# Performance work log

Measured on AMD Instinct MI355X. Metric: run time of the kernel, lower is better.

Reference implementation:

```python
import jax, jax.numpy as jnp
import numpy as np

B = 32768   # batch (agents)
H = 64      # h_dim
E = 16      # embedding_dim
M = 6       # num_modes (n_samples)
P = M * 2   # traj_points
T = 30      # pred_len (seq_len)


def setup_inputs() -> dict:
    key = jax.random.key(0)
    ks = jax.random.split(key, 14)
    def s(k, shape, scale=0.1):
        return jax.random.normal(k, shape, jnp.float32) * scale
    return dict(
        traj_abs=s(ks[0], (1, B, 2), 1.0),
        traj_rel=s(ks[1], (1, B, 2), 1.0),
        h0=s(ks[2], (1, B, H)),
        c0=s(ks[3], (1, B, H)),
        W_ih=s(ks[4], (4 * H, E)),
        W_hh=s(ks[5], (4 * H, H)),
        b_ih=s(ks[6], (4 * H,)),
        b_hh=s(ks[7], (4 * H,)),
        W_se=s(ks[8], (E, P)),
        b_se=s(ks[9], (E,)),
        W_pos=s(ks[10], (P, H)),
        b_pos=s(ks[11], (P,)),
        W_conf=s(ks[12], (M, H)),
        b_conf=s(ks[13], (M,)),
    )


def reference(traj_abs, traj_rel, h0, c0, W_ih, W_hh, b_ih, b_hh,
              W_se, b_se, W_pos, b_pos, W_conf, b_conf):
    b = traj_rel.shape[1]
    # repeat_interleave the (x,y) pair num_modes times along feature dim -> [b, 12]
    rel12 = jnp.tile(traj_rel.reshape(b, 1, 2), (1, M, 1)).reshape(b, P)
    x = jax.nn.leaky_relu(rel12 @ W_se.T + b_se)  # [b, E]
    h = h0[0]
    c = c0[0]

    def step(carry, _):
        x, h, c = carry
        # PyTorch LSTM cell, gate order i, f, g, o
        gates = x @ W_ih.T + b_ih + h @ W_hh.T + b_hh  # [b, 4H]
        i, f, g, o = jnp.split(gates, 4, axis=-1)
        c = jax.nn.sigmoid(f) * c + jax.nn.sigmoid(i) * jnp.tanh(g)
        h = jax.nn.sigmoid(o) * jnp.tanh(c)
        rel = h @ W_pos.T + b_pos                      # [b, P]
        x = jax.nn.leaky_relu(rel @ W_se.T + b_se)     # [b, E]
        return (x, h, c), rel

    (x, h, c), rels = jax.lax.scan(step, (x, h, c), None, length=T)  # rels: [T, b, P]
    pred = rels.reshape(T, b, M, 2).transpose(1, 2, 0, 3)            # [b, M, T, 2]
    conf = jax.nn.softmax(h @ W_conf.T + b_conf, axis=1)             # [b, M]
    return pred, conf
```

## Files before the change

kernel.cpp:

```cpp
#include <hip/hip_runtime.h>
#include <hip/hip_bf16.h>

typedef _Float16 half8 __attribute__((ext_vector_type(8)));
typedef _Float16 half4 __attribute__((ext_vector_type(4)));
typedef float float4v __attribute__((ext_vector_type(4)));

#define BATCH 32768
#define TT 30

#if __has_builtin(__builtin_amdgcn_exp2f)
#define FEXP2(x) __builtin_amdgcn_exp2f(x)
#else
#define FEXP2(x) __expf((x) * 0.6931471805599453f)
#endif
#if __has_builtin(__builtin_amdgcn_rcpf)
#define FRCP(x) __builtin_amdgcn_rcpf(x)
#else
#define FRCP(x) (1.0f / (x))
#endif

#define NLOG2E  -1.4426950408889634f
#define N2LOG2E -2.8853900817779268f

#define WFRAG_OFF 0
#define WCF_OFF   12288
#define BIASB_OFF 13312
#define SXY_OFF   13568
#define CBIAS_OFF 13616
#define WCONF_OFF 13648
#define BCONF_OFF 14032
#define FLAG_IDX  14038
#define CONF_BASE (BATCH * 360)

__global__ void detect_kernel(const unsigned short* __restrict__ raw,
                              int* __restrict__ flag_out) {
    __shared__ int sflag[256];
    int local = 0;
    for (int i = threadIdx.x; i < 16384; i += 256) {
        unsigned short u = raw[i];
        if ((u & 0x7F80u) == 0x7F80u) local = 1;
    }
    sflag[threadIdx.x] = local;
    __syncthreads();
    if (threadIdx.x == 0) {
        int f = 0;
        for (int i = 0; i < 256; ++i) f |= sflag[i];
        flag_out[0] = f;
    }
}

__device__ __forceinline__ float ldin(const void* p, int i, int isf32) {
    return isf32 ? ((const float*)p)[i]
                 : (float)((const __hip_bfloat16*)p)[i];
}

__global__ void prep_kernel(const void* __restrict__ W_ih,
                            const void* __restrict__ W_hh,
                            const void* __restrict__ b_ih,
                            const void* __restrict__ b_hh,
                            const void* __restrict__ W_se,
                            const void* __restrict__ b_se,
                            const void* __restrict__ W_pos,
                            const void* __restrict__ b_pos,
                            const void* __restrict__ W_conf,
                            const void* __restrict__ b_conf,
                            float* __restrict__ ws)
{
    const int isf32 = ((const int*)(ws + FLAG_IDX))[0];
    int tid = blockIdx.x * blockDim.x + threadIdx.x;
    int stride = gridDim.x * blockDim.x;
    _Float16* wfh = (_Float16*)ws;

    for (int idx = tid; idx < 24576; idx += stride) {
        int jj = idx & 7, r = idx >> 3;
        int lane = r & 63; r >>= 6;
        int ks = r % 3; r /= 3;
        int gate = r & 3; int wv = r >> 2;
        int col = lane & 15, akq = lane >> 4;
        int k = ks * 32 + akq * 8 + jj;
        int row = gate * 64 + wv * 16 + col;
        float v = 0.f;
        if (k < 16) v = ldin(W_ih, row * 16 + k, isf32);
        else if (k < 80) v = ldin(W_hh, row * 64 + (k - 16), isf32);
        v *= (gate == 2) ? N2LOG2E : NLOG2E;
        wfh[idx] = (_Float16)v;
    }
    _Float16* wch = (_Float16*)(ws + WCF_OFF);
    for (int idx = tid; idx < 2048; idx += stride) {
        int jj = idx & 7, r = idx >> 3;
        int lane = r & 63; r >>= 6;
        int ks = r & 1, role = r >> 1;
        int col = lane & 15, akq = lane >> 4;
        int k = ks * 32 + akq * 8 + jj;
        float v = 0.f;
        if (role == 0) {
            if (col < 12) v = ldin(W_pos, col * 64 + k, isf32);
        } else {
            float s = 0.f;
            for (int p = 0; p < 12; ++p)
                s += ldin(W_se, col * 12 + p, isf32) * ldin(W_pos, p * 64 + k, isf32);
            v = s;
        }
        wch[idx] = (_Float16)v;
    }
    for (int idx = tid; idx < 256; idx += stride) {
        int gate = idx >> 6;
        float scale = (gate == 2) ? N2LOG2E : NLOG2E;
        ws[BIASB_OFF + idx] = (ldin(b_ih, idx, isf32) + ldin(b_hh, idx, isf32)) * scale;
    }
    for (int idx = tid; idx < 16; idx += stride) {
        float sx = 0.f, sy = 0.f;
        for (int m = 0; m < 6; ++m) {
            sx += ldin(W_se, idx * 12 + 2 * m, isf32);
            sy += ldin(W_se, idx * 12 + 2 * m + 1, isf32);
        }
        ws[SXY_OFF + idx * 3 + 0] = sx;
        ws[SXY_OFF + idx * 3 + 1] = sy;
        ws[SXY_OFF + idx * 3 + 2] = ldin(b_se, idx, isf32);
    }
    for (int idx = tid; idx < 32; idx += stride) {
        int w = idx >> 4, cc = idx & 15;
        float v = 0.f;
        if (w == 0) {
            if (cc < 12) v = ldin(b_pos, cc, isf32);
        } else {
            float s = ldin(b_se, cc, isf32);
            for (int p = 0; p < 12; ++p)
                s += ldin(W_se, cc * 12 + p, isf32) * ldin(b_pos, p, isf32);
            v = s;
        }
        ws[CBIAS_OFF + idx] = v;
    }
    for (int idx = tid; idx < 384; idx += stride)
        ws[WCONF_OFF + idx] = ldin(W_conf, idx, isf32);
    for (int idx = tid; idx < 6; idx += stride)
        ws[BCONF_OFF + idx] = ldin(b_conf, idx, isf32);
}

__global__ __launch_bounds__(256, 4) void lstm_kernel(
    const void* __restrict__ traj_rel,
    const void* __restrict__ h0,
    const void* __restrict__ c0,
    const float* __restrict__ ws,
    float* __restrict__ out)
{
    __shared__ _Float16 zsh[2 * 16 * 104];
    __shared__ _Float16 predh[12 * 30 * 36];

    const int tid = threadIdx.x;
    const int lane = tid & 63;
    const int wid = __builtin_amdgcn_readfirstlane(tid >> 6);
    const int role = wid & 1;
    const int col16 = lane & 15;
    const int akq = lane >> 4;
    const int base = blockIdx.x * 32;
    const int isf32 = ((const int*)(ws + FLAG_IDX))[0];

    const float4v* wfg = (const float4v*)ws;
    half8 Bf[4][3];
#pragma unroll
    for (int tl = 0; tl < 4; ++tl)
#pragma unroll
        for (int ks = 0; ks < 3; ++ks)
            Bf[tl][ks] = __builtin_bit_cast(half8,
                wfg[((wid * 4 + tl) * 3 + ks) * 64 + lane]);
    float bias4[4];
#pragma unroll
    for (int tl = 0; tl < 4; ++tl)
        bias4[tl] = ws[BIASB_OFF + tl * 64 + wid * 16 + col16];
    half8 wfc[2];
    {
        const float4v* wcg = (const float4v*)(ws + WCF_OFF);
#pragma unroll
        for (int ks = 0; ks < 2; ++ks)
            wfc[ks] = __builtin_bit_cast(half8, wcg[(role * 2 + ks) * 64 + lane]);
    }
    const float cb = ws[CBIAS_OFF + role * 16 + col16];

    float cg0[4], cg1[4];
    {
        int unit = wid * 16 + col16;
#pragma unroll
        for (int i = 0; i < 4; ++i) {
            cg0[i] = ldin(c0, (base + akq * 4 + i) * 64 + unit, isf32);
            cg1[i] = ldin(c0, (base + 16 + akq * 4 + i) * 64 + unit, isf32);
        }
    }
    {
        int m = tid & 31, jq2 = tid >> 5;
        int g = m >> 4, row = m & 15;
        _Float16* zg = &zsh[g * 1664];
        half8 ha;
#pragma unroll
        for (int i = 0; i < 8; ++i)
            ha[i] = (_Float16)ldin(h0, (base + m) * 64 + jq2 * 8 + i, isf32);
        *(half8*)&zg[row * 104 + 16 + jq2 * 8] = ha;
        if (jq2 < 4) {
            float rx = ldin(traj_rel, 2 * (base + m), isf32);
            float ry = ldin(traj_rel, 2 * (base + m) + 1, isf32);
            half4 xs;
#pragma unroll
            for (int i = 0; i < 4; ++i) {
                int e = 4 * jq2 + i;
                float x = fmaf(rx, ws[SXY_OFF + e * 3],
                          fmaf(ry, ws[SXY_OFF + e * 3 + 1], ws[SXY_OFF + e * 3 + 2]));
                xs[i] = (_Float16)(x > 0.f ? x : 0.01f * x);
            }
            *(half4*)&zg[row * 104 + 4 * jq2] = xs;
        } else if (jq2 < 6) {
            half8 zz = {};
            *(half8*)&zg[row * 104 + 80 + (jq2 - 4) * 8] = zz;
        }
    }
    __syncthreads();

    const int zbA = col16 * 104 + akq * 8;
    const int zbC = zbA + 16;
    const int hwb = 16 + wid * 16 + col16;

    float4v acc0[4], acc1[4];

#define ZG(g) (&zsh[(g) * 1664])

#define PHASE_A(G, ACC) do {                                                  \
    _Float16* zg_ = ZG(G);                                                    \
    _Pragma("unroll")                                                         \
    for (int tl = 0; tl < 4; ++tl) {                                          \
        float bv = bias4[tl];                                                 \
        ACC[tl][0] = bv; ACC[tl][1] = bv; ACC[tl][2] = bv; ACC[tl][3] = bv;   \
    }                                                                         \
    _Pragma("unroll")                                                         \
    for (int ks = 0; ks < 3; ++ks) {                                          \
        half8 af_ = *(const half8*)&zg_[zbA + ks * 32];                       \
        _Pragma("unroll")                                                     \
        for (int tl = 0; tl < 4; ++tl)                                        \
            ACC[tl] = __builtin_amdgcn_mfma_f32_16x16x32_f16(                 \
                af_, Bf[tl][ks], ACC[tl], 0, 0, 0);                           \
    }                                                                         \
} while (0)

#define PHASE_B(G, ACC, CARR) do {                                            \
    _Float16* zg_ = ZG(G);                                                    \
    _Pragma("unroll")                                                         \
    for (int i = 0; i < 4; ++i) {                                             \
        float si = FRCP(1.0f + FEXP2(ACC[0][i]));                             \
        float sf = FRCP(1.0f + FEXP2(ACC[1][i]));                             \
        float tg = fmaf(2.0f, FRCP(1.0f + FEXP2(ACC[2][i])), -1.0f);          \
        float so = FRCP(1.0f + FEXP2(ACC[3][i]));                             \
        float cn = fmaf(sf, CARR[i], si * tg);                                \
        CARR[i] = cn;                                                         \
        float th = fmaf(2.0f, FRCP(1.0f + FEXP2(cn * N2LOG2E)), -1.0f);       \
        float hn = so * th;                                                   \
        zg_[(akq * 4 + i) * 104 + hwb] = (_Float16)hn;                        \
    }                                                                         \
} while (0)

#define PHASE_C(G, T) do {                                                    \
    _Float16* zg_ = ZG(G);                                                    \
    float4v racc_;                                                            \
    racc_[0] = cb; racc_[1] = cb; racc_[2] = cb; racc_[3] = cb;               \
    _Pragma("unroll")                                                         \
    for (int ks = 0; ks < 2; ++ks) {                                          \
        half8 af_ = *(const half8*)&zg_[zbC + ks * 32];                       \
        racc_ = __builtin_amdgcn_mfma_f32_16x16x32_f16(                       \
            af_, wfc[ks], racc_, 0, 0, 0);                                    \
    }                                                                         \
    if (role == 0) {                                                          \
        if (col16 < 12) {                                                     \
            half4 hv_;                                                        \
            _Pragma("unroll")                                                 \
            for (int i = 0; i < 4; ++i) hv_[i] = (_Float16)racc_[i];          \
            *(half4*)&predh[(col16 * 30 + (T)) * 36 + (G) * 16 + akq * 4] = hv_; \
        }                                                                     \
    } else if ((T) != TT - 1) {                                               \
        _Pragma("unroll")                                                     \
        for (int i = 0; i < 4; ++i) {                                         \
            float xv_ = racc_[i];                                             \
            xv_ = xv_ > 0.f ? xv_ : 0.01f * xv_;                              \
            zg_[(akq * 4 + i) * 104 + col16] = (_Float16)xv_;                 \
        }                                                                     \
    }                                                                         \
} while (0)

    PHASE_A(0, acc0);
    __syncthreads();
    PHASE_A(1, acc1); PHASE_B(0, acc0, cg0);
    __syncthreads();
    if (wid < 2) PHASE_C(0, 0);
    PHASE_B(1, acc1, cg1);
    __syncthreads();

    for (int t = 1; t < TT; ++t) {
        PHASE_A(0, acc0);
        if (wid >= 2) PHASE_C(1, t - 1);
        __syncthreads();
        PHASE_A(1, acc1); PHASE_B(0, acc0, cg0);
        __syncthreads();
        if (wid < 2) PHASE_C(0, t);
        PHASE_B(1, acc1, cg1);
        __syncthreads();
    }
    if (wid >= 2) PHASE_C(1, TT - 1);
    __syncthreads();

    {
        float4* po4 = (float4*)(out + (size_t)base * 360);
#pragma unroll 1
        for (int q2 = 0; q2 < 12; ++q2) {
            int idx4 = q2 * 256 + tid;
            if (idx4 < 2880) {
                int a = idx4 / 90, rem = idx4 % 90;
                int m = rem / 15, tq = rem % 15;
                int t0 = tq * 2;
                float4 o;
                o.x = (float)predh[((2 * m + 0) * 30 + t0) * 36 + a];
                o.y = (float)predh[((2 * m + 1) * 30 + t0) * 36 + a];
                o.z = (float)predh[((2 * m + 0) * 30 + t0 + 1) * 36 + a];
                o.w = (float)predh[((2 * m + 1) * 30 + t0 + 1) * 36 + a];
                po4[idx4] = o;
            }
        }
    }

    if (wid == 0 && lane < 32) {
        int m = lane;
        int g = m >> 4, row = m & 15;
        float l[6];
#pragma unroll
        for (int md = 0; md < 6; ++md) l[md] = ws[BCONF_OFF + md];
        for (int jj = 0; jj < 64; ++jj) {
            float hv = (float)zsh[g * 1664 + row * 104 + 16 + jj];
#pragma unroll
            for (int md = 0; md < 6; ++md)
                l[md] = fmaf(hv, ws[WCONF_OFF + md * 64 + jj], l[md]);
        }
        float mx = l[0];
#pragma unroll
        for (int md = 1; md < 6; ++md) mx = fmaxf(mx, l[md]);
        float ex[6], s = 0.f;
#pragma unroll
        for (int md = 0; md < 6; ++md) { ex[md] = __expf(l[md] - mx); s += ex[md]; }
        float inv = FRCP(s);
#pragma unroll
        for (int md = 0; md < 6; ++md)
            out[CONF_BASE + (size_t)(base + m) * 6 + md] = ex[md] * inv;
    }
}

extern "C" void kernel_launch(void* const* d_in, const int* in_sizes, int n_in,
                              void* d_out, int out_size, void* d_ws, size_t ws_size,
                              hipStream_t stream) {
    const void* traj_rel = d_in[1];
    const void* h0   = d_in[2];
    const void* c0   = d_in[3];
    const void* W_ih = d_in[4];
    const void* W_hh = d_in[5];
    const void* b_ih = d_in[6];
    const void* b_hh = d_in[7];
    const void* W_se = d_in[8];
    const void* b_se = d_in[9];
    const void* W_pos  = d_in[10];
    const void* b_pos  = d_in[11];
    const void* W_conf = d_in[12];
    const void* b_conf = d_in[13];
    float* ws = (float*)d_ws;
    float* out = (float*)d_out;

    detect_kernel<<<1, 256, 0, stream>>>((const unsigned short*)W_hh,
                                         (int*)(ws + FLAG_IDX));
    prep_kernel<<<40, 256, 0, stream>>>(W_ih, W_hh, b_ih, b_hh, W_se, b_se,
                                        W_pos, b_pos, W_conf, b_conf, ws);
    lstm_kernel<<<BATCH / 32, 256, 0, stream>>>(traj_rel, h0, c0, ws, out);
}
```

Baseline: 207.9 us.

## Double-buffer LSTM hidden state in LDS, fuse gate phases, and cut barriers per step

Each row of the shared z buffer now holds two hidden-state slots, so a step can write the new h into one slot while other waves still read the old h from the other. This lets the gate MFMA and the activation phase be fused into one PHASE_AB and removes one __syncthreads per timestep. The loop is unrolled by two to alternate slots. The activation math is also recombined to use fewer reciprocals by sharing denominators (sigmoid/tanh products folded into one rcp). The cost is a larger LDS footprint and more complex index arithmetic, plus some risk of overflow in the combined exponent products.

```diff
diff --git a/kernel.cpp b/kernel.cpp
--- a/kernel.cpp
+++ b/kernel.cpp
@@ -144,7 +144,7 @@
     const float* __restrict__ ws,
     float* __restrict__ out)
 {
-    __shared__ _Float16 zsh[2 * 16 * 104];
+    __shared__ _Float16 zsh[2 * 16 * 168];
     __shared__ _Float16 predh[12 * 30 * 36];
 
     const int tid = threadIdx.x;
@@ -177,6 +177,21 @@
     }
     const float cb = ws[CBIAS_OFF + role * 16 + col16];
 
+    int aoff[2][3];
+#pragma unroll
+    for (int p = 0; p < 2; ++p)
+#pragma unroll
+        for (int ks = 0; ks < 3; ++ks) {
+            int q = ks * 4 + akq;
+            int off = (q < 2) ? q * 8
+                    : (q < 10) ? 32 + p * 64 + (q - 2) * 8
+                               : 16 + (q - 10) * 8;
+            aoff[p][ks] = col16 * 168 + off;
+        }
+    const int zcb = col16 * 168 + 32 + akq * 8;
+    const int rb = akq * 672;
+    const int hb = 32 + wid * 16 + col16;
+
     float cg0[4], cg1[4];
     {
         int unit = wid * 16 + col16;
@@ -189,12 +204,12 @@
     {
         int m = tid & 31, jq2 = tid >> 5;
         int g = m >> 4, row = m & 15;
-        _Float16* zg = &zsh[g * 1664];
+        _Float16* zg = &zsh[g * 2688 + row * 168];
         half8 ha;
 #pragma unroll
         for (int i = 0; i < 8; ++i)
             ha[i] = (_Float16)ldin(h0, (base + m) * 64 + jq2 * 8 + i, isf32);
-        *(half8*)&zg[row * 104 + 16 + jq2 * 8] = ha;
+        *(half8*)&zg[32 + jq2 * 8] = ha;
         if (jq2 < 4) {
             float rx = ldin(traj_rel, 2 * (base + m), isf32);
             float ry = ldin(traj_rel, 2 * (base + m) + 1, isf32);
@@ -206,62 +221,54 @@
                           fmaf(ry, ws[SXY_OFF + e * 3 + 1], ws[SXY_OFF + e * 3 + 2]));
                 xs[i] = (_Float16)(x > 0.f ? x : 0.01f * x);
             }
-            *(half4*)&zg[row * 104 + 4 * jq2] = xs;
+            *(half4*)&zg[4 * jq2] = xs;
         } else if (jq2 < 6) {
             half8 zz = {};
-            *(half8*)&zg[row * 104 + 80 + (jq2 - 4) * 8] = zz;
-        }
-    }
-    __syncthreads();
-
-    const int zbA = col16 * 104 + akq * 8;
-    const int zbC = zbA + 16;
-    const int hwb = 16 + wid * 16 + col16;
-
-    float4v acc0[4], acc1[4];
-
-#define ZG(g) (&zsh[(g) * 1664])
-
-#define PHASE_A(G, ACC) do {                                                  \
-    _Float16* zg_ = ZG(G);                                                    \
+            *(half8*)&zg[16 + (jq2 - 4) * 8] = zz;
+        }
+    }
+    __syncthreads();
+
+    _Float16* const zg0p = &zsh[0];
+    _Float16* const zg1p = &zsh[2688];
+
+#define PHASE_AB(ZG, PC, PN, CARR) do {                                       \
+    float4v acc_[4];                                                          \
     _Pragma("unroll")                                                         \
     for (int tl = 0; tl < 4; ++tl) {                                          \
         float bv = bias4[tl];                                                 \
-        ACC[tl][0] = bv; ACC[tl][1] = bv; ACC[tl][2] = bv; ACC[tl][3] = bv;   \
+        acc_[tl][0] = bv; acc_[tl][1] = bv; acc_[tl][2] = bv; acc_[tl][3] = bv;\
     }                                                                         \
     _Pragma("unroll")                                                         \
     for (int ks = 0; ks < 3; ++ks) {                                          \
-        half8 af_ = *(const half8*)&zg_[zbA + ks * 32];                       \
+        half8 af_ = *(const half8*)&(ZG)[aoff[PC][ks]];                       \
         _Pragma("unroll")                                                     \
         for (int tl = 0; tl < 4; ++tl)                                        \
-            ACC[tl] = __builtin_amdgcn_mfma_f32_16x16x32_f16(                 \
-                af_, Bf[tl][ks], ACC[tl], 0, 0, 0);                           \
-    }                                                                         \
-} while (0)
-
-#define PHASE_B(G, ACC, CARR) do {                                            \
-    _Float16* zg_ = ZG(G);                                                    \
+            acc_[tl] = __builtin_amdgcn_mfma_f32_16x16x32_f16(                \
+                af_, Bf[tl][ks], acc_[tl], 0, 0, 0);                          \
+    }                                                                         \
     _Pragma("unroll")                                                         \
     for (int i = 0; i < 4; ++i) {                                             \
-        float si = FRCP(1.0f + FEXP2(ACC[0][i]));                             \
-        float sf = FRCP(1.0f + FEXP2(ACC[1][i]));                             \
-        float tg = fmaf(2.0f, FRCP(1.0f + FEXP2(ACC[2][i])), -1.0f);          \
-        float so = FRCP(1.0f + FEXP2(ACC[3][i]));                             \
-        float cn = fmaf(sf, CARR[i], si * tg);                                \
-        CARR[i] = cn;                                                         \
-        float th = fmaf(2.0f, FRCP(1.0f + FEXP2(cn * N2LOG2E)), -1.0f);       \
-        float hn = so * th;                                                   \
-        zg_[(akq * 4 + i) * 104 + hwb] = (_Float16)hn;                        \
+        float ei = FEXP2(acc_[0][i]);                                         \
+        float ef = FEXP2(acc_[1][i]);                                         \
+        float eg = FEXP2(acc_[2][i]);                                         \
+        float eo = FEXP2(acc_[3][i]);                                         \
+        float pp = (1.f + ei) * (1.f + eg);                                   \
+        float qq = 1.f + ef;                                                  \
+        float cn = fmaf((CARR)[i], pp, (1.f - eg) * qq) * FRCP(pp * qq);      \
+        (CARR)[i] = cn;                                                       \
+        float ec = FEXP2(cn * N2LOG2E);                                       \
+        float hn = (1.f - ec) * FRCP((1.f + eo) * (1.f + ec));                \
+        (ZG)[rb + i * 168 + (PN) * 64 + hb] = (_Float16)hn;                   \
     }                                                                         \
 } while (0)
 
-#define PHASE_C(G, T) do {                                                    \
-    _Float16* zg_ = ZG(G);                                                    \
+#define PHASE_C(ZG, P, T, GI) do {                                            \
     float4v racc_;                                                            \
     racc_[0] = cb; racc_[1] = cb; racc_[2] = cb; racc_[3] = cb;               \
     _Pragma("unroll")                                                         \
     for (int ks = 0; ks < 2; ++ks) {                                          \
-        half8 af_ = *(const half8*)&zg_[zbC + ks * 32];                       \
+        half8 af_ = *(const half8*)&(ZG)[zcb + (P) * 64 + ks * 32];           \
         racc_ = __builtin_amdgcn_mfma_f32_16x16x32_f16(                       \
             af_, wfc[ks], racc_, 0, 0, 0);                                    \
     }                                                                         \
@@ -270,37 +277,45 @@
             half4 hv_;                                                        \
             _Pragma("unroll")                                                 \
             for (int i = 0; i < 4; ++i) hv_[i] = (_Float16)racc_[i];          \
-            *(half4*)&predh[(col16 * 30 + (T)) * 36 + (G) * 16 + akq * 4] = hv_; \
+            *(half4*)&predh[(col16 * 30 + (T)) * 36 + (GI) * 16 + akq * 4] = hv_;\
         }                                                                     \
     } else if ((T) != TT - 1) {                                               \
         _Pragma("unroll")                                                     \
         for (int i = 0; i < 4; ++i) {                                         \
             float xv_ = racc_[i];                                             \
             xv_ = xv_ > 0.f ? xv_ : 0.01f * xv_;                              \
-            zg_[(akq * 4 + i) * 104 + col16] = (_Float16)xv_;                 \
+            (ZG)[rb + i * 168 + col16] = (_Float16)xv_;                       \
         }                                                                     \
     }                                                                         \
 } while (0)
 
-    PHASE_A(0, acc0);
-    __syncthreads();
-    PHASE_A(1, acc1); PHASE_B(0, acc0, cg0);
-    __syncthreads();
-    if (wid < 2) PHASE_C(0, 0);
-    PHASE_B(1, acc1, cg1);
-    __syncthreads();
-
-    for (int t = 1; t < TT; ++t) {
-        PHASE_A(0, acc0);
-        if (wid >= 2) PHASE_C(1, t - 1);
+    PHASE_AB(zg0p, 0, 1, cg0);
+    __syncthreads();
+    PHASE_AB(zg1p, 0, 1, cg1);
+    if (wid < 2) PHASE_C(zg0p, 1, 0, 0);
+    __syncthreads();
+
+    for (int t = 1; t < TT - 1; t += 2) {
+        PHASE_AB(zg0p, 1, 0, cg0);
+        if (wid >= 2) PHASE_C(zg1p, 1, t - 1, 1);
         __syncthreads();
-        PHASE_A(1, acc1); PHASE_B(0, acc0, cg0);
+        PHASE_AB(zg1p, 1, 0, cg1);
+        if (wid < 2) PHASE_C(zg0p, 0, t, 0);
         __syncthreads();
-        if (wid < 2) PHASE_C(0, t);
-        PHASE_B(1, acc1, cg1);
+        PHASE_AB(zg0p, 0, 1, cg0);
+        if (wid >= 2) PHASE_C(zg1p, 0, t, 1);
         __syncthreads();
-    }
-    if (wid >= 2) PHASE_C(1, TT - 1);
+        PHASE_AB(zg1p, 0, 1, cg1);
+        if (wid < 2) PHASE_C(zg0p, 1, t + 1, 0);
+        __syncthreads();
+    }
+    PHASE_AB(zg0p, 1, 0, cg0);
+    if (wid >= 2) PHASE_C(zg1p, 1, TT - 2, 1);
+    __syncthreads();
+    PHASE_AB(zg1p, 1, 0, cg1);
+    if (wid < 2) PHASE_C(zg0p, 0, TT - 1, 0);
+    __syncthreads();
+    if (wid >= 2) PHASE_C(zg1p, 0, TT - 1, 1);
     __syncthreads();
 
     {
@@ -329,7 +344,7 @@
 #pragma unroll
         for (int md = 0; md < 6; ++md) l[md] = ws[BCONF_OFF + md];
         for (int jj = 0; jj < 64; ++jj) {
-            float hv = (float)zsh[g * 1664 + row * 104 + 16 + jj];
+            float hv = (float)zsh[g * 2688 + row * 168 + 32 + jj];
 #pragma unroll
             for (int md = 0; md < 6; ++md)
                 l[md] = fmaf(hv, ws[WCONF_OFF + md * 64 + jj], l[md]);
```

New measurement: 196.8 us. -5.3%, faster.
